# Optimization experiments

Hardware: AMD Instinct MI355X
Metric: run time of the kernel (lower is better)

Reference implementation:

```python
import jax, jax.numpy as jnp
from jax import lax
import numpy as np

# ---- config (repo globals, scaled to a 112x112 feature map of a 448 image) ----
IMG, FEAT = 448, 112
PSTRIDE = IMG // FEAT  # 4 pixels per feature cell
RATIOS = [(16, 16), (12, 20), (20, 12),
          (24, 24), (20, 28), (28, 20),
          (32, 32), (24, 40), (40, 24), (28, 40), (40, 28), (28, 36), (36, 28)]
GROUPS = [(0, 3), (3, 6), (6, 13)]   # ratio groups per NMS scale
N_LIST = [2, 3, 2]
IOU_THRESHS = [0.25, 0.25, 0.25]
BATCH = 256
WINDOW_NUMS = [(FEAT - rh + 1) * (FEAT - rw + 1) for rh, rw in RATIOS]
TOTAL = sum(WINDOW_NUMS)             # 96981
PROPOSALN = sum(N_LIST)              # 7


def _coordinates():
    # Mirrors ComputeCoordinate: box = [x0,y0,x1,y1] in pixels, lefttop clipped to 0.
    parts = []
    for rh, rw in RATIOS:
        nr, nc = FEAT - rh + 1, FEAT - rw + 1
        xi = np.repeat(np.arange(nr), nc).astype(np.float32)
        yi = np.tile(np.arange(nc), nr).astype(np.float32)
        x0 = xi * PSTRIDE - 1.0
        y0 = yi * PSTRIDE - 1.0
        x1 = x0 + rh * PSTRIDE
        y1 = y0 + rw * PSTRIDE
        x0 = np.maximum(x0, 0.0)
        y0 = np.maximum(y0, 0.0)
        parts.append(np.stack([x0, y0, x1, y1], 1))
    return np.concatenate(parts, 0).astype(np.float32)  # (TOTAL, 4)


def setup_inputs() -> dict:
    key = jax.random.key(0)
    x = jax.random.normal(key, (BATCH, 1, FEAT, FEAT), jnp.float32)
    coords = jnp.asarray(_coordinates())
    return {"x": x, "coords": coords, "proposalN": PROPOSALN}


def _nms(scores, coords, n_pick, thresh):
    # Greedy NMS: repeatedly take best-scoring alive window, suppress IoU > thresh.
    # If everything is suppressed before n_pick picks, repeat the last pick (repo behavior).
    areas = (coords[:, 2] - coords[:, 0] + 1.0) * (coords[:, 3] - coords[:, 1] + 1.0)

    def step(state, _):
        alive, last = state
        any_alive = jnp.any(alive)
        idx = jnp.where(any_alive,
                        jnp.argmax(jnp.where(alive, scores, -jnp.inf)).astype(jnp.int32),
                        last)
        box = coords[idx]
        lt = jnp.maximum(coords[:, :2], box[:2])
        rb = jnp.minimum(coords[:, 2:], box[2:])
        w = rb[:, 0] - lt[:, 0] + 1.0
        h = rb[:, 1] - lt[:, 1] + 1.0
        inter = jnp.where((w < 0) | (h < 0), 0.0, w * h)
        iou = inter / (areas + areas[idx] - inter)
        keep = (alive & (iou <= thresh)).at[idx].set(False)
        return (jnp.where(any_alive, keep, alive), idx), idx

    init = (jnp.ones(scores.shape[0], bool), jnp.int32(0))
    return lax.scan(step, init, None, length=n_pick)[1]  # (n_pick,) int32


def _forward(x, coords):
    B = x.shape[0]
    # multiscale sliding-window average scores (AvgPool2d, stride 1, VALID)
    avgs = [lax.reduce_window(x, 0.0, lax.add, (1, 1, rh, rw), (1, 1, 1, 1), 'VALID')
            .reshape(B, -1) / float(rh * rw) for rh, rw in RATIOS]
    all_scores = jnp.concatenate(avgs, 1)  # (B, TOTAL)

    idx_parts = []
    for j, (g0, g1) in enumerate(GROUPS):
        s0 = int(sum(WINDOW_NUMS[:g0]))
        s1 = int(sum(WINDOW_NUMS[:g1]))
        cd = coords[s0:s1]
        nms_j = lambda s, cd=cd, j=j: _nms(s, cd, N_LIST[j], IOU_THRESHS[j])
        picks = jax.vmap(nms_j)(all_scores[:, s0:s1])  # (B, N_LIST[j])
        idx_parts.append(picks + s0)
    proposalN_indices = jnp.concatenate(idx_parts, 1)  # (B, PROPOSALN)
    proposalN_windows_scores = jnp.take_along_axis(all_scores, proposalN_indices, 1)
    window_scores = all_scores  # reshape(batch, -1) of all_scores
    return proposalN_indices, proposalN_windows_scores, window_scores


def reference(x, coords, proposalN):
    assert proposalN == PROPOSALN
    return _forward(x, coords)
```

## Files before the change

kernel.cpp:

```cpp
#include <hip/hip_runtime.h>
#include <math.h>
#include <limits.h>

namespace {
constexpr int kFeat = 112;
constexpr int kBatch = 256;
constexpr int kTotal = 96981;
constexpr int kStride = 116;
constexpr int kNT = 512;
constexpr int kRH[13] = {16,12,20,24,20,28,32,24,40,28,40,28,36};
constexpr int kRW[13] = {16,20,12,24,28,20,32,40,24,40,28,36,28};
constexpr int kOff[13] = {0,9409,18802,28195,36116,44021,51926,58487,64984,71481,77686,83891,90436};
constexpr int kNQY[13] = {25,24,26,23,22,24,21,19,23,19,22,20,22};
constexpr int kNQ[13]  = {2425,2424,2418,2047,2046,2040,1701,1691,1679,1615,1606,1700,1694};
constexpr int kNB[13]  = {38,38,38,32,32,32,27,27,27,26,26,27,27};
constexpr int kNBMax = 187;

constexpr int nb_sum(int RB, int RE) {
  int s = 0;
  for (int r = RB; r < RE; ++r) s += kNB[r];
  return s;
}
}

__device__ __forceinline__ float* pad_score(float* sat, int e) {
  return sat + (e / 3) * kStride + 113 + (e % 3);
}
__device__ __forceinline__ unsigned char* pad_local(float* sat, int e) {
  const int i = 4 * kNBMax + e;
  const int r = i / 12;
  return (unsigned char*)sat + r * (kStride * 4) + 113 * 4 + (i - r * 12);
}

struct NmsShared {
  float rs[kNT / 64];
  int   ri[kNT / 64];
  float shS; int shI;
  float pX0[3], pY0[3], pX1[3], pY1[3], pA[3];
  unsigned long long dirtyM[kNT / 64];
};

__device__ __forceinline__ void block_argmax(float s, int i, NmsShared* ns) {
  __syncthreads();
#pragma unroll
  for (int off = 32; off > 0; off >>= 1) {
    const float s2 = __shfl_down(s, off, 64);
    const int   i2 = __shfl_down(i, off, 64);
    if (s2 > s || (s2 == s && i2 < i)) { s = s2; i = i2; }
  }
  const int wave = threadIdx.x >> 6;
  if ((threadIdx.x & 63) == 0) { ns->rs[wave] = s; ns->ri[wave] = i; }
  __syncthreads();
  if (threadIdx.x == 0) {
    float bs = ns->rs[0]; int bi = ns->ri[0];
#pragma unroll
    for (int w = 1; w < kNT / 64; ++w)
      if (ns->rs[w] > bs || (ns->rs[w] == bs && ns->ri[w] < bi)) { bs = ns->rs[w]; bi = ns->ri[w]; }
    ns->shS = bs; ns->shI = bi;
  }
  __syncthreads();
}

__device__ void build_sat(const float* __restrict__ xb, float* __restrict__ sat) {
  const int tid = threadIdx.x;
  for (int j = tid; j < kStride; j += kNT) sat[j] = 0.f;
  for (int r = tid; r < 113; r += kNT) sat[r * kStride] = 0.f;
  const float4* x4 = (const float4*)xb;
  for (int i = tid; i < (kFeat * kFeat) / 4; i += kNT) {
    const float4 v = x4[i];
    const int r = i / (kFeat / 4);
    const int c = (i - r * (kFeat / 4)) * 4;
    float* dst = sat + (r + 1) * kStride + c + 1;
    dst[0] = v.x; dst[1] = v.y; dst[2] = v.z; dst[3] = v.w;
  }
  __syncthreads();
  const int wave = tid >> 6, lane = tid & 63;
  for (int r = 1 + wave; r <= kFeat; r += kNT / 64) {
    float* row = sat + r * kStride;
    float v = row[1 + lane];
#pragma unroll
    for (int d = 1; d < 64; d <<= 1) { const float u = __shfl_up(v, d, 64); if (lane >= d) v += u; }
    row[1 + lane] = v;
    const float tot = __shfl(v, 63, 64);
    const int c = 65 + lane;
    float w = (c <= kFeat) ? row[c] : 0.f;
#pragma unroll
    for (int d = 1; d < 64; d <<= 1) { const float u = __shfl_up(w, d, 64); if (lane >= d) w += u; }
    if (c <= kFeat) row[c] = w + tot;
  }
  __syncthreads();
  const int seg = tid / kFeat;
  const int col = tid - seg * kFeat + 1;
  if (tid < 4 * kFeat) {
    const int r0 = seg * 28 + 1;
    float s = 0.f;
    for (int r = r0; r < r0 + 28; ++r) { s += sat[r * kStride + col]; sat[r * kStride + col] = s; }
  }
  __syncthreads();
  float off = 0.f;
  if (tid < 4 * kFeat && seg > 0) {
#pragma unroll
    for (int s2 = 1; s2 <= 3; ++s2)
      if (s2 <= seg) off += sat[(28 * s2) * kStride + col];
  }
  __syncthreads();
  if (tid < 4 * kFeat && seg > 0) {
    const int r0 = seg * 28 + 1;
    for (int r = r0; r < r0 + 28; ++r) sat[r * kStride + col] += off;
  }
  __syncthreads();
}

template<int RB, int RE>
__device__ __forceinline__ void decode_geom(int pi, float& x0, float& y0,
                                            float& x1, float& y1, float& a) {
  x0 = 0.f; y0 = 0.f; x1 = 0.f; y1 = 0.f; a = 0.f;
#pragma unroll
  for (int rr = RB; rr < RE; ++rr) {
    const int nr = kFeat - kRH[rr] + 1, nc = kFeat - kRW[rr] + 1;
    if (pi >= kOff[rr] && pi < kOff[rr] + nr * nc) {
      const int l = pi - kOff[rr];
      const int xi = l / nc, yi = l - xi * nc;
      const float x0u = xi * 4.0f - 1.0f, y0u = yi * 4.0f - 1.0f;
      x1 = x0u + kRH[rr] * 4.0f; y1 = y0u + kRW[rr] * 4.0f;
      x0 = fmaxf(x0u, 0.0f); y0 = fmaxf(y0u, 0.0f);
      a = (x1 - x0 + 1.0f) * (y1 - y0 + 1.0f);
    }
  }
}

template<int RB, int RE>
__device__ __forceinline__ void entry_geom(float* sat, int e, float& x0, float& y0,
                                           float& x1, float& y1, float& a) {
  const int local = (int)*pad_local(sat, e);
  x0 = 0.f; y0 = 0.f; x1 = 0.f; y1 = 0.f; a = 0.f;
  int eb = 0;
#pragma unroll
  for (int rr = RB; rr < RE; ++rr) {
    if (e >= eb && e < eb + kNB[rr]) {
      const int nqy = kNQY[rr], nc = kFeat - kRW[rr] + 1;
      const int qb = (e - eb) << 6;
      const int bxi = qb / nqy;
      const int gi = kOff[rr] + bxi * nc + ((qb - bxi * nqy) << 2) + local;
      const int l = gi - kOff[rr];
      const int xi = l / nc, yi = l - xi * nc;
      const float x0u = xi * 4.0f - 1.0f, y0u = yi * 4.0f - 1.0f;
      x1 = x0u + kRH[rr] * 4.0f; y1 = y0u + kRW[rr] * 4.0f;
      x0 = fmaxf(x0u, 0.0f); y0 = fmaxf(y0u, 0.0f);
      a = (x1 - x0 + 1.0f) * (y1 - y0 + 1.0f);
    }
    eb += kNB[rr];
  }
}

template<int RB, int RE>
__device__ __forceinline__ void pick_store(float* sat, NmsShared* ns, int k, int slot,
                                           float* __restrict__ out_idx,
                                           float* __restrict__ out_sc, int b) {
  if (threadIdx.x == 0) {
    const int e = ns->shI;
    const int local = (int)*pad_local(sat, e);
    int gi = 0, ebase = 0;
#pragma unroll
    for (int rr = RB; rr < RE; ++rr) {
      if (e >= ebase && e < ebase + kNB[rr]) {
        const int nqy = kNQY[rr], nc = kFeat - kRW[rr] + 1;
        const int qb = (e - ebase) << 6;
        const int bxi = qb / nqy;
        gi = kOff[rr] + bxi * nc + ((qb - bxi * nqy) << 2) + local;
      }
      ebase += kNB[rr];
    }
    float x0, y0, x1, y1, a;
    decode_geom<RB, RE>(gi, x0, y0, x1, y1, a);
    ns->pX0[k] = x0; ns->pY0[k] = y0; ns->pX1[k] = x1; ns->pY1[k] = y1; ns->pA[k] = a;
    out_idx[b * 7 + slot + k] = (float)gi;
    out_sc [b * 7 + slot + k] = ns->shS;
  }
  __syncthreads();
}

template<int RB, int RE, int NP>
__device__ __forceinline__ void rescan_block(float* sat, NmsShared* ns, int e, int k,
                                             int lane) {
  int ebase = 0;
#pragma unroll
  for (int rr = RB; rr < RE; ++rr) {
    if (e >= ebase && e < ebase + kNB[rr]) {
      const int rh = kRH[rr], rw = kRW[rr];
      const int nc = kFeat - rw + 1;
      const int nqy = kNQY[rr];
      const int NQ = kNQ[rr];
      const float inv = 1.0f / (float)(rh * rw);
      const int q = ((e - ebase) << 6) + lane;
      const bool act = q < NQ;
      const int qc = act ? q : NQ - 1;
      const int xi = qc / nqy, qy = qc - xi * nqy;
      const int yi0 = qy << 2;
      const float* u = sat + xi * kStride;
      const float* d = u + rh * kStride;
      const float4 U0 = *(const float4*)(u + yi0);
      const float4 U1 = *(const float4*)(u + yi0 + rw);
      const float4 D0 = *(const float4*)(d + yi0);
      const float4 D1 = *(const float4*)(d + yi0 + rw);
      float s4[4];
      s4[0] = (D1.x - U1.x - D0.x + U0.x) * inv;
      s4[1] = (D1.y - U1.y - D0.y + U0.y) * inv;
      s4[2] = (D1.z - U1.z - D0.z + U0.z) * inv;
      s4[3] = (D1.w - U1.w - D0.w + U0.w) * inv;
      const float X0u = xi * 4.0f - 1.0f;
      const float X1 = X0u + rh * 4.0f;
      const float X0 = fmaxf(X0u, 0.0f);
      const float Ax = X1 - X0 + 1.0f;
      float wxp[NP > 1 ? NP - 1 : 1];
#pragma unroll
      for (int p = 0; p < NP - 1; ++p)
        if (p < k) wxp[p] = fminf(X1, ns->pX1[p]) - fmaxf(X0, ns->pX0[p]) + 1.0f;
      const int gi0 = kOff[rr] + xi * nc + yi0;
      const int rem = nc - yi0;
      float bs = -INFINITY; int bgi = INT_MAX;
      if (act) {
#pragma unroll
        for (int j = 0; j < 4; ++j) {
          if (j >= rem) break;
          const float Y0u = (yi0 + j) * 4.0f - 1.0f;
          const float Y1 = Y0u + rw * 4.0f;
          const float Y0 = fmaxf(Y0u, 0.0f);
          const float A = Ax * (Y1 - Y0 + 1.0f);
          bool alive = true;
#pragma unroll
          for (int p = 0; p < NP - 1; ++p) {
            if (p >= k) break;
            const float hyp = fminf(Y1, ns->pY1[p]) - fmaxf(Y0, ns->pY0[p]) + 1.0f;
            alive &= !((wxp[p] >= 0.0f) & (hyp >= 0.0f) &
                       (5.0f * wxp[p] * hyp > A + ns->pA[p]));
          }
          if (alive && s4[j] > bs) { bs = s4[j]; bgi = gi0 + j; }
        }
      }
      float wm = bs;
#pragma unroll
      for (int off = 32; off > 0; off >>= 1) wm = fmaxf(wm, __shfl_down(wm, off, 64));
      wm = __shfl(wm, 0, 64);
      const unsigned long long bal = __ballot(bs == wm);
      if (lane == __ffsll(bal) - 1) {
        const int qbB = (e - ebase) << 6;
        const int bxiB = qbB / nqy;
        const int giBase = kOff[rr] + bxiB * nc + ((qbB - bxiB * nqy) << 2);
        *pad_score(sat, e) = wm;
        *pad_local(sat, e) =
            (unsigned char)((bgi == INT_MAX) ? 0 : (bgi - giBase));
      }
    }
    ebase += kNB[rr];
  }
}

template<int RB, int RE, int NP, int SLOT>
__device__ void run_group(float* sat, NmsShared* ns,
                          float* __restrict__ wb,
                          float* __restrict__ out_idx, float* __restrict__ out_sc, int b) {
  constexpr int NBtot = nb_sum(RB, RE);
  const int tid = threadIdx.x;
  const int lane = tid & 63;
  const int wave = tid >> 6;

  int eb = 0;
#pragma unroll
  for (int rr = RB; rr < RE; ++rr) {
    const int rh = kRH[rr], rw = kRW[rr];
    const int nc = kFeat - rw + 1;
    const int nqy = kNQY[rr];
    const int NQ = kNQ[rr];
    const float inv = 1.0f / (float)(rh * rw);
    for (int qb = (tid & ~63); qb < NQ; qb += kNT) {
      const int q = qb + lane;
      const bool act = q < NQ;
      const int qc = act ? q : NQ - 1;
      const int xi = qc / nqy, qy = qc - xi * nqy;
      const int yi0 = qy << 2;
      const float* u = sat + xi * kStride;
      const float* d = u + rh * kStride;
      const float4 U0 = *(const float4*)(u + yi0);
      const float4 U1 = *(const float4*)(u + yi0 + rw);
      const float4 D0 = *(const float4*)(d + yi0);
      const float4 D1 = *(const float4*)(d + yi0 + rw);
      const float s0 = (D1.x - U1.x - D0.x + U0.x) * inv;
      const float s1 = (D1.y - U1.y - D0.y + U0.y) * inv;
      const float s2 = (D1.z - U1.z - D0.z + U0.z) * inv;
      const float s3 = (D1.w - U1.w - D0.w + U0.w) * inv;
      const int gi0 = kOff[rr] + xi * nc + yi0;
      const int rem = nc - yi0;
      float bs = -INFINITY; int bgi = INT_MAX;
      if (act) {
        float* w = wb + gi0;
        w[0] = s0; bs = s0; bgi = gi0;
        if (rem > 1) { w[1] = s1; if (s1 > bs) { bs = s1; bgi = gi0 + 1; } }
        if (rem > 2) { w[2] = s2; if (s2 > bs) { bs = s2; bgi = gi0 + 2; } }
        if (rem > 3) { w[3] = s3; if (s3 > bs) { bs = s3; bgi = gi0 + 3; } }
      }
      float wm = bs;
#pragma unroll
      for (int off = 32; off > 0; off >>= 1) wm = fmaxf(wm, __shfl_down(wm, off, 64));
      wm = __shfl(wm, 0, 64);
      const unsigned long long bal = __ballot(bs == wm);
      if (lane == __ffsll(bal) - 1) {
        const int e = eb + (qb >> 6);
        const int bxi = qb / nqy;
        const int giBase = kOff[rr] + bxi * nc + ((qb - bxi * nqy) << 2);
        *pad_score(sat, e) = wm;
        *pad_local(sat, e) = (unsigned char)(bgi - giBase);
      }
    }
    eb += kNB[rr];
  }
  __syncthreads();

  {
    const float s = (tid < NBtot) ? *pad_score(sat, tid) : -INFINITY;
    const int   i = (tid < NBtot) ? tid : INT_MAX;
    block_argmax(s, i, ns);
  }
  pick_store<RB, RE>(sat, ns, 0, SLOT, out_idx, out_sc, b);

  for (int k = 1; k < NP; ++k) {
    const float nx0 = ns->pX0[k-1], ny0 = ns->pY0[k-1];
    const float nx1 = ns->pX1[k-1], ny1 = ns->pY1[k-1], na = ns->pA[k-1];

    bool sup = false;
    if (tid < NBtot) {
      const float es = *pad_score(sat, tid);
      if (es != -INFINITY) {
        float x0, y0, x1, y1, a;
        entry_geom<RB, RE>(sat, tid, x0, y0, x1, y1, a);
        const float twx = fminf(x1, nx1) - fmaxf(x0, nx0) + 1.0f;
        const float thy = fminf(y1, ny1) - fmaxf(y0, ny0) + 1.0f;
        sup = (twx >= 0.0f) & (thy >= 0.0f) & (5.0f * twx * thy > a + na);
      }
    }
    const unsigned long long m0 = __ballot(sup);
    if (lane == 0) ns->dirtyM[wave] = m0;
    __syncthreads();

    int cnt = 0;
#pragma unroll
    for (int wm = 0; wm < kNT / 64; ++wm) {
      unsigned long long m = ns->dirtyM[wm];
      while (m) {
        const int bit = __ffsll(m) - 1;
        m &= m - 1;
        if ((cnt & 7) == wave) {
          rescan_block<RB, RE, NP>(sat, ns, (wm << 6) + bit, k, lane);
        }
        ++cnt;
      }
    }
    __syncthreads();

    {
      const float s = (tid < NBtot) ? *pad_score(sat, tid) : -INFINITY;
      const int   i = (tid < NBtot) ? tid : INT_MAX;
      block_argmax(s, i, ns);
    }
    pick_store<RB, RE>(sat, ns, k, SLOT, out_idx, out_sc, b);
  }
}

__global__ __launch_bounds__(kNT, 6) void appm_fused(const float* __restrict__ x,
                                                     float* __restrict__ win,
                                                     float* __restrict__ out_idx,
                                                     float* __restrict__ out_sc) {
  __shared__ __align__(16) float sat[113 * kStride];
  __shared__ NmsShared ns;
  const int b = blockIdx.x / 3;
  const int t = blockIdx.x % 3;

  build_sat(x + (size_t)b * kFeat * kFeat, sat);

  float* wb = win + (size_t)b * kTotal;
  if (t == 0)       run_group<0, 3, 2, 0>(sat, &ns, wb, out_idx, out_sc, b);
  else if (t == 1)  run_group<3, 6, 3, 2>(sat, &ns, wb, out_idx, out_sc, b);
  else              run_group<6, 13, 2, 5>(sat, &ns, wb, out_idx, out_sc, b);
}

extern "C" void kernel_launch(void* const* d_in, const int* in_sizes, int n_in,
                              void* d_out, int out_size, void* d_ws, size_t ws_size,
                              hipStream_t stream) {
  const float* x = (const float*)d_in[0];
  float* out     = (float*)d_out;
  float* out_idx = out;
  float* out_sc  = out + kBatch * 7;
  float* win     = out + 2 * kBatch * 7;

  appm_fused<<<kBatch * 3, kNT, 0, stream>>>(x, win, out_idx, out_sc);
}
```

Before: 164.3 us.

## Coarsen NMS block-max entries to 256 windows-groups with 16-bit local index

Each block-max summary entry now covers four 64-quad chunks (up to 1024 windows) instead of one, which cuts the entry count per ratio from 26-38 to 7-10. The local argmax offset is stored as a 16-bit value, and the wave reduction now carries the index with a tie-break, replacing the ballot. This shrinks the per-pick suppression check and the block argmax over entries. In exchange, each dirty entry rescan covers four times as many windows, and each wave in the initial pass loops over four chunks.

Result: no change. 166.6 us (+1.3%).

```diff
diff --git a/kernel.cpp b/kernel.cpp
--- a/kernel.cpp
+++ b/kernel.cpp
@@ -13,12 +13,11 @@
 constexpr int kOff[13] = {0,9409,18802,28195,36116,44021,51926,58487,64984,71481,77686,83891,90436};
 constexpr int kNQY[13] = {25,24,26,23,22,24,21,19,23,19,22,20,22};
 constexpr int kNQ[13]  = {2425,2424,2418,2047,2046,2040,1701,1691,1679,1615,1606,1700,1694};
-constexpr int kNB[13]  = {38,38,38,32,32,32,27,27,27,26,26,27,27};
-constexpr int kNBMax = 187;
-
-constexpr int nb_sum(int RB, int RE) {
+constexpr int kNE[13]  = {10,10,10,8,8,8,7,7,7,7,7,7,7};
+
+constexpr int ne_sum(int RB, int RE) {
   int s = 0;
-  for (int r = RB; r < RE; ++r) s += kNB[r];
+  for (int r = RB; r < RE; ++r) s += kNE[r];
   return s;
 }
 }
@@ -26,10 +25,10 @@
 __device__ __forceinline__ float* pad_score(float* sat, int e) {
   return sat + (e / 3) * kStride + 113 + (e % 3);
 }
-__device__ __forceinline__ unsigned char* pad_local(float* sat, int e) {
-  const int i = 4 * kNBMax + e;
-  const int r = i / 12;
-  return (unsigned char*)sat + r * (kStride * 4) + 113 * 4 + (i - r * 12);
+__device__ __forceinline__ unsigned short* pad_local16(float* sat, int e) {
+  const int p = 256 + 2 * e;
+  const int r = p / 12;
+  return (unsigned short*)((char*)sat + r * (kStride * 4) + 113 * 4 + (p - r * 12));
 }
 
 struct NmsShared {
@@ -130,27 +129,20 @@
 }
 
 template<int RB, int RE>
-__device__ __forceinline__ void entry_geom(float* sat, int e, float& x0, float& y0,
-                                           float& x1, float& y1, float& a) {
-  const int local = (int)*pad_local(sat, e);
-  x0 = 0.f; y0 = 0.f; x1 = 0.f; y1 = 0.f; a = 0.f;
-  int eb = 0;
+__device__ __forceinline__ int entry_gi(float* sat, int e) {
+  const int local = (int)*pad_local16(sat, e);
+  int gi = 0, eb = 0;
 #pragma unroll
   for (int rr = RB; rr < RE; ++rr) {
-    if (e >= eb && e < eb + kNB[rr]) {
+    if (e >= eb && e < eb + kNE[rr]) {
       const int nqy = kNQY[rr], nc = kFeat - kRW[rr] + 1;
-      const int qb = (e - eb) << 6;
-      const int bxi = qb / nqy;
-      const int gi = kOff[rr] + bxi * nc + ((qb - bxi * nqy) << 2) + local;
-      const int l = gi - kOff[rr];
-      const int xi = l / nc, yi = l - xi * nc;
-      const float x0u = xi * 4.0f - 1.0f, y0u = yi * 4.0f - 1.0f;
-      x1 = x0u + kRH[rr] * 4.0f; y1 = y0u + kRW[rr] * 4.0f;
-      x0 = fmaxf(x0u, 0.0f); y0 = fmaxf(y0u, 0.0f);
-      a = (x1 - x0 + 1.0f) * (y1 - y0 + 1.0f);
-    }
-    eb += kNB[rr];
-  }
+      const int qb0 = (e - eb) << 8;
+      const int bxi = qb0 / nqy;
+      gi = kOff[rr] + bxi * nc + ((qb0 - bxi * nqy) << 2) + local;
+    }
+    eb += kNE[rr];
+  }
+  return gi;
 }
 
 template<int RB, int RE>
@@ -158,19 +150,7 @@
                                            float* __restrict__ out_idx,
                                            float* __restrict__ out_sc, int b) {
   if (threadIdx.x == 0) {
-    const int e = ns->shI;
-    const int local = (int)*pad_local(sat, e);
-    int gi = 0, ebase = 0;
-#pragma unroll
-    for (int rr = RB; rr < RE; ++rr) {
-      if (e >= ebase && e < ebase + kNB[rr]) {
-        const int nqy = kNQY[rr], nc = kFeat - kRW[rr] + 1;
-        const int qb = (e - ebase) << 6;
-        const int bxi = qb / nqy;
-        gi = kOff[rr] + bxi * nc + ((qb - bxi * nqy) << 2) + local;
-      }
-      ebase += kNB[rr];
-    }
+    const int gi = entry_gi<RB, RE>(sat, ns->shI);
     float x0, y0, x1, y1, a;
     decode_geom<RB, RE>(gi, x0, y0, x1, y1, a);
     ns->pX0[k] = x0; ns->pY0[k] = y0; ns->pX1[k] = x1; ns->pY1[k] = y1; ns->pA[k] = a;
@@ -181,78 +161,85 @@
 }
 
 template<int RB, int RE, int NP>
-__device__ __forceinline__ void rescan_block(float* sat, NmsShared* ns, int e, int k,
+__device__ __forceinline__ void rescan_entry(float* sat, NmsShared* ns, int e, int k,
                                              int lane) {
   int ebase = 0;
 #pragma unroll
   for (int rr = RB; rr < RE; ++rr) {
-    if (e >= ebase && e < ebase + kNB[rr]) {
+    if (e >= ebase && e < ebase + kNE[rr]) {
       const int rh = kRH[rr], rw = kRW[rr];
       const int nc = kFeat - rw + 1;
       const int nqy = kNQY[rr];
       const int NQ = kNQ[rr];
       const float inv = 1.0f / (float)(rh * rw);
-      const int q = ((e - ebase) << 6) + lane;
-      const bool act = q < NQ;
-      const int qc = act ? q : NQ - 1;
-      const int xi = qc / nqy, qy = qc - xi * nqy;
-      const int yi0 = qy << 2;
-      const float* u = sat + xi * kStride;
-      const float* d = u + rh * kStride;
-      const float4 U0 = *(const float4*)(u + yi0);
-      const float4 U1 = *(const float4*)(u + yi0 + rw);
-      const float4 D0 = *(const float4*)(d + yi0);
-      const float4 D1 = *(const float4*)(d + yi0 + rw);
-      float s4[4];
-      s4[0] = (D1.x - U1.x - D0.x + U0.x) * inv;
-      s4[1] = (D1.y - U1.y - D0.y + U0.y) * inv;
-      s4[2] = (D1.z - U1.z - D0.z + U0.z) * inv;
-      s4[3] = (D1.w - U1.w - D0.w + U0.w) * inv;
-      const float X0u = xi * 4.0f - 1.0f;
-      const float X1 = X0u + rh * 4.0f;
-      const float X0 = fmaxf(X0u, 0.0f);
-      const float Ax = X1 - X0 + 1.0f;
-      float wxp[NP > 1 ? NP - 1 : 1];
-#pragma unroll
-      for (int p = 0; p < NP - 1; ++p)
-        if (p < k) wxp[p] = fminf(X1, ns->pX1[p]) - fmaxf(X0, ns->pX0[p]) + 1.0f;
-      const int gi0 = kOff[rr] + xi * nc + yi0;
-      const int rem = nc - yi0;
+      const int eL = e - ebase;
       float bs = -INFINITY; int bgi = INT_MAX;
-      if (act) {
-#pragma unroll
-        for (int j = 0; j < 4; ++j) {
-          if (j >= rem) break;
-          const float Y0u = (yi0 + j) * 4.0f - 1.0f;
-          const float Y1 = Y0u + rw * 4.0f;
-          const float Y0 = fmaxf(Y0u, 0.0f);
-          const float A = Ax * (Y1 - Y0 + 1.0f);
-          bool alive = true;
-#pragma unroll
-          for (int p = 0; p < NP - 1; ++p) {
-            if (p >= k) break;
-            const float hyp = fminf(Y1, ns->pY1[p]) - fmaxf(Y0, ns->pY0[p]) + 1.0f;
-            alive &= !((wxp[p] >= 0.0f) & (hyp >= 0.0f) &
-                       (5.0f * wxp[p] * hyp > A + ns->pA[p]));
+#pragma unroll
+      for (int c = 0; c < 4; ++c) {
+        const int qb = ((eL << 2) + c) << 6;
+        if (qb >= NQ) break;
+        const int q = qb + lane;
+        const bool act = q < NQ;
+        const int qc = act ? q : NQ - 1;
+        const int xi = qc / nqy, qy = qc - xi * nqy;
+        const int yi0 = qy << 2;
+        const float* u = sat + xi * kStride;
+        const float* d = u + rh * kStride;
+        const float4 U0 = *(const float4*)(u + yi0);
+        const float4 U1 = *(const float4*)(u + yi0 + rw);
+        const float4 D0 = *(const float4*)(d + yi0);
+        const float4 D1 = *(const float4*)(d + yi0 + rw);
+        float s4[4];
+        s4[0] = (D1.x - U1.x - D0.x + U0.x) * inv;
+        s4[1] = (D1.y - U1.y - D0.y + U0.y) * inv;
+        s4[2] = (D1.z - U1.z - D0.z + U0.z) * inv;
+        s4[3] = (D1.w - U1.w - D0.w + U0.w) * inv;
+        const float X0u = xi * 4.0f - 1.0f;
+        const float X1 = X0u + rh * 4.0f;
+        const float X0 = fmaxf(X0u, 0.0f);
+        const float Ax = X1 - X0 + 1.0f;
+        float wxp[NP > 1 ? NP - 1 : 1];
+#pragma unroll
+        for (int p = 0; p < NP - 1; ++p)
+          if (p < k) wxp[p] = fminf(X1, ns->pX1[p]) - fmaxf(X0, ns->pX0[p]) + 1.0f;
+        const int gi0 = kOff[rr] + xi * nc + yi0;
+        const int rem = nc - yi0;
+        if (act) {
+#pragma unroll
+          for (int j = 0; j < 4; ++j) {
+            if (j >= rem) break;
+            const float Y0u = (yi0 + j) * 4.0f - 1.0f;
+            const float Y1 = Y0u + rw * 4.0f;
+            const float Y0 = fmaxf(Y0u, 0.0f);
+            const float A = Ax * (Y1 - Y0 + 1.0f);
+            bool alive = true;
+#pragma unroll
+            for (int p = 0; p < NP - 1; ++p) {
+              if (p >= k) break;
+              const float hyp = fminf(Y1, ns->pY1[p]) - fmaxf(Y0, ns->pY0[p]) + 1.0f;
+              alive &= !((wxp[p] >= 0.0f) & (hyp >= 0.0f) &
+                         (5.0f * wxp[p] * hyp > A + ns->pA[p]));
+            }
+            if (alive && s4[j] > bs) { bs = s4[j]; bgi = gi0 + j; }
           }
-          if (alive && s4[j] > bs) { bs = s4[j]; bgi = gi0 + j; }
         }
       }
-      float wm = bs;
-#pragma unroll
-      for (int off = 32; off > 0; off >>= 1) wm = fmaxf(wm, __shfl_down(wm, off, 64));
-      wm = __shfl(wm, 0, 64);
-      const unsigned long long bal = __ballot(bs == wm);
-      if (lane == __ffsll(bal) - 1) {
-        const int qbB = (e - ebase) << 6;
-        const int bxiB = qbB / nqy;
-        const int giBase = kOff[rr] + bxiB * nc + ((qbB - bxiB * nqy) << 2);
-        *pad_score(sat, e) = wm;
-        *pad_local(sat, e) =
-            (unsigned char)((bgi == INT_MAX) ? 0 : (bgi - giBase));
-      }
-    }
-    ebase += kNB[rr];
+#pragma unroll
+      for (int off = 32; off > 0; off >>= 1) {
+        const float s2 = __shfl_down(bs, off, 64);
+        const int   i2 = __shfl_down(bgi, off, 64);
+        if (s2 > bs || (s2 == bs && i2 < bgi)) { bs = s2; bgi = i2; }
+      }
+      if (lane == 0) {
+        const int qb0 = eL << 8;
+        const int bxi = qb0 / nqy;
+        const int giBase = kOff[rr] + bxi * nc + ((qb0 - bxi * nqy) << 2);
+        *pad_score(sat, e) = bs;
+        *pad_local16(sat, e) =
+            (unsigned short)((bgi == INT_MAX) ? 0 : (bgi - giBase));
+      }
+    }
+    ebase += kNE[rr];
   }
 }
 
@@ -260,7 +247,7 @@
 __device__ void run_group(float* sat, NmsShared* ns,
                           float* __restrict__ wb,
                           float* __restrict__ out_idx, float* __restrict__ out_sc, int b) {
-  constexpr int NBtot = nb_sum(RB, RE);
+  constexpr int NEtot = ne_sum(RB, RE);
   const int tid = threadIdx.x;
   const int lane = tid & 63;
   const int wave = tid >> 6;
@@ -272,53 +259,60 @@
     const int nc = kFeat - rw + 1;
     const int nqy = kNQY[rr];
     const int NQ = kNQ[rr];
+    const int NE = kNE[rr];
     const float inv = 1.0f / (float)(rh * rw);
-    for (int qb = (tid & ~63); qb < NQ; qb += kNT) {
-      const int q = qb + lane;
-      const bool act = q < NQ;
-      const int qc = act ? q : NQ - 1;
-      const int xi = qc / nqy, qy = qc - xi * nqy;
-      const int yi0 = qy << 2;
-      const float* u = sat + xi * kStride;
-      const float* d = u + rh * kStride;
-      const float4 U0 = *(const float4*)(u + yi0);
-      const float4 U1 = *(const float4*)(u + yi0 + rw);
-      const float4 D0 = *(const float4*)(d + yi0);
-      const float4 D1 = *(const float4*)(d + yi0 + rw);
-      const float s0 = (D1.x - U1.x - D0.x + U0.x) * inv;
-      const float s1 = (D1.y - U1.y - D0.y + U0.y) * inv;
-      const float s2 = (D1.z - U1.z - D0.z + U0.z) * inv;
-      const float s3 = (D1.w - U1.w - D0.w + U0.w) * inv;
-      const int gi0 = kOff[rr] + xi * nc + yi0;
-      const int rem = nc - yi0;
+    for (int e = wave; e < NE; e += kNT / 64) {
       float bs = -INFINITY; int bgi = INT_MAX;
-      if (act) {
-        float* w = wb + gi0;
-        w[0] = s0; bs = s0; bgi = gi0;
-        if (rem > 1) { w[1] = s1; if (s1 > bs) { bs = s1; bgi = gi0 + 1; } }
-        if (rem > 2) { w[2] = s2; if (s2 > bs) { bs = s2; bgi = gi0 + 2; } }
-        if (rem > 3) { w[3] = s3; if (s3 > bs) { bs = s3; bgi = gi0 + 3; } }
-      }
-      float wm = bs;
-#pragma unroll
-      for (int off = 32; off > 0; off >>= 1) wm = fmaxf(wm, __shfl_down(wm, off, 64));
-      wm = __shfl(wm, 0, 64);
-      const unsigned long long bal = __ballot(bs == wm);
-      if (lane == __ffsll(bal) - 1) {
-        const int e = eb + (qb >> 6);
-        const int bxi = qb / nqy;
-        const int giBase = kOff[rr] + bxi * nc + ((qb - bxi * nqy) << 2);
-        *pad_score(sat, e) = wm;
-        *pad_local(sat, e) = (unsigned char)(bgi - giBase);
-      }
-    }
-    eb += kNB[rr];
+#pragma unroll
+      for (int c = 0; c < 4; ++c) {
+        const int qb = ((e << 2) + c) << 6;
+        if (qb >= NQ) break;
+        const int q = qb + lane;
+        const bool act = q < NQ;
+        const int qc = act ? q : NQ - 1;
+        const int xi = qc / nqy, qy = qc - xi * nqy;
+        const int yi0 = qy << 2;
+        const float* u = sat + xi * kStride;
+        const float* d = u + rh * kStride;
+        const float4 U0 = *(const float4*)(u + yi0);
+        const float4 U1 = *(const float4*)(u + yi0 + rw);
+        const float4 D0 = *(const float4*)(d + yi0);
+        const float4 D1 = *(const float4*)(d + yi0 + rw);
+        const float s0 = (D1.x - U1.x - D0.x + U0.x) * inv;
+        const float s1 = (D1.y - U1.y - D0.y + U0.y) * inv;
+        const float s2 = (D1.z - U1.z - D0.z + U0.z) * inv;
+        const float s3 = (D1.w - U1.w - D0.w + U0.w) * inv;
+        const int gi0 = kOff[rr] + xi * nc + yi0;
+        const int rem = nc - yi0;
+        if (act) {
+          float* w = wb + gi0;
+          w[0] = s0; if (s0 > bs) { bs = s0; bgi = gi0; }
+          if (rem > 1) { w[1] = s1; if (s1 > bs) { bs = s1; bgi = gi0 + 1; } }
+          if (rem > 2) { w[2] = s2; if (s2 > bs) { bs = s2; bgi = gi0 + 2; } }
+          if (rem > 3) { w[3] = s3; if (s3 > bs) { bs = s3; bgi = gi0 + 3; } }
+        }
+      }
+#pragma unroll
+      for (int off = 32; off > 0; off >>= 1) {
+        const float s2 = __shfl_down(bs, off, 64);
+        const int   i2 = __shfl_down(bgi, off, 64);
+        if (s2 > bs || (s2 == bs && i2 < bgi)) { bs = s2; bgi = i2; }
+      }
+      if (lane == 0) {
+        const int qb0 = e << 8;
+        const int bxi = qb0 / nqy;
+        const int giBase = kOff[rr] + bxi * nc + ((qb0 - bxi * nqy) << 2);
+        *pad_score(sat, eb + e) = bs;
+        *pad_local16(sat, eb + e) = (unsigned short)(bgi - giBase);
+      }
+    }
+    eb += kNE[rr];
   }
   __syncthreads();
 
   {
-    const float s = (tid < NBtot) ? *pad_score(sat, tid) : -INFINITY;
-    const int   i = (tid < NBtot) ? tid : INT_MAX;
+    const float s = (tid < NEtot) ? *pad_score(sat, tid) : -INFINITY;
+    const int   i = (tid < NEtot) ? tid : INT_MAX;
     block_argmax(s, i, ns);
   }
   pick_store<RB, RE>(sat, ns, 0, SLOT, out_idx, out_sc, b);
@@ -328,11 +322,12 @@
     const float nx1 = ns->pX1[k-1], ny1 = ns->pY1[k-1], na = ns->pA[k-1];
 
     bool sup = false;
-    if (tid < NBtot) {
+    if (tid < NEtot) {
       const float es = *pad_score(sat, tid);
       if (es != -INFINITY) {
+        const int gi = entry_gi<RB, RE>(sat, tid);
         float x0, y0, x1, y1, a;
-        entry_geom<RB, RE>(sat, tid, x0, y0, x1, y1, a);
+        decode_geom<RB, RE>(gi, x0, y0, x1, y1, a);
         const float twx = fminf(x1, nx1) - fmaxf(x0, nx0) + 1.0f;
         const float thy = fminf(y1, ny1) - fmaxf(y0, ny0) + 1.0f;
         sup = (twx >= 0.0f) & (thy >= 0.0f) & (5.0f * twx * thy > a + na);
@@ -350,7 +345,7 @@
         const int bit = __ffsll(m) - 1;
         m &= m - 1;
         if ((cnt & 7) == wave) {
-          rescan_block<RB, RE, NP>(sat, ns, (wm << 6) + bit, k, lane);
+          rescan_entry<RB, RE, NP>(sat, ns, (wm << 6) + bit, k, lane);
         }
         ++cnt;
       }
@@ -358,8 +353,8 @@
     __syncthreads();
 
     {
-      const float s = (tid < NBtot) ? *pad_score(sat, tid) : -INFINITY;
-      const int   i = (tid < NBtot) ? tid : INT_MAX;
+      const float s = (tid < NEtot) ? *pad_score(sat, tid) : -INFINITY;
+      const int   i = (tid < NEtot) ? tid : INT_MAX;
       block_argmax(s, i, ns);
     }
     pick_store<RB, RE>(sat, ns, k, SLOT, out_idx, out_sc, b);
```
